# Kernel optimization log

Hardware: AMD Instinct MI355X
Metric: run time of the kernel (lower is better)

Reference implementation:

```python
import jax, jax.numpy as jnp
import numpy as np

NEG_INF = -jnp.inf


def setup_inputs() -> dict:
    key = jax.random.key(0)
    ks = jax.random.split(key, 20)
    B, N, M = 8, 1024, 128
    F_OP, F_MA, F_E, OUT, HID = 64, 64, 16, 64, 128
    inp = {
        "x": jax.random.normal(ks[0], (B, N, F_OP), dtype=jnp.float32),
        "y": jax.random.normal(ks[1], (B, M, F_MA), dtype=jnp.float32),
        "z": jax.random.normal(ks[2], (B, N, M, F_E), dtype=jnp.float32),
        "op_adj_in": jax.random.randint(ks[3], (B, N, N), 0, 2, dtype=jnp.int32),
        "ma_adj_in": jax.random.randint(ks[4], (B, N, N), 0, 2, dtype=jnp.int32),
        "op_ma_adj": jax.random.randint(ks[5], (B, N, M), 0, 2, dtype=jnp.int32),
        # learned parameters
        "weight_op": jax.random.normal(ks[6], (F_OP, OUT), dtype=jnp.float32) * 0.1,
        "weight_ma": jax.random.normal(ks[7], (F_MA, OUT), dtype=jnp.float32) * 0.1,
        "weight_edge": jax.random.normal(ks[8], (F_E, OUT), dtype=jnp.float32) * 0.1,
        "attention_op": jax.random.normal(ks[9], (1, 2 * OUT), dtype=jnp.float32) * 0.1,
        "attention_ma": jax.random.normal(ks[10], (1, 3 * OUT), dtype=jnp.float32) * 0.1,
        "w1": jax.random.normal(ks[11], (2 * OUT, HID), dtype=jnp.float32) * 0.1,
        "b1": jnp.zeros((HID,), dtype=jnp.float32),
        "w2": jax.random.normal(ks[12], (HID, HID), dtype=jnp.float32) * 0.1,
        "b2": jnp.zeros((HID,), dtype=jnp.float32),
        "wo": jax.random.normal(ks[13], (HID, OUT), dtype=jnp.float32) * 0.1,
        "bo": jnp.zeros((OUT,), dtype=jnp.float32),
    }
    return inp


def reference(x, y, z, op_adj_in, ma_adj_in, op_ma_adj,
              weight_op, weight_ma, weight_edge, attention_op, attention_ma,
              w1, b1, w2, b2, wo, bo):
    OUT = weight_op.shape[1]
    h = jnp.einsum('bni,io->bno', x, weight_op)  # [B,N,OUT]
    # all_combinations[b,i,j] = cat(h[b,j], h[b,i]); dot with attention_op splits:
    a1 = attention_op[0, :OUT]
    a2 = attention_op[0, OUT:]
    e_op = (h @ a2)[:, :, None] + (h @ a1)[:, None, :]  # [B,N,N]
    e_op = jax.nn.leaky_relu(e_op, negative_slope=0.01)

    adj = (jnp.swapaxes(op_adj_in, 1, 2) + op_adj_in
           + jnp.swapaxes(ma_adj_in, 1, 2) + ma_adj_in)  # [B,N,N]
    row_mask = jnp.all(op_ma_adj == 0, axis=-1)  # [B,N] ops with no machine link
    adj = jnp.where(row_mask[:, :, None], 1, adj)
    att = jnp.where(adj > 0, e_op, NEG_INF)
    attention_in_op = jax.nn.softmax(att, axis=2)
    h_prime_op = jnp.einsum('bij,bjo->bio', attention_in_op, h)  # [B,N,OUT]

    h_ma = jnp.einsum('bmi,io->bmo', y, weight_ma)  # [B,M,OUT]
    h_edge = jnp.einsum('bnmi,io->bnmo', z, weight_edge)  # [B,N,M,OUT]
    # cat([h_op_i, h_ma_j, h_edge_ij]) @ attention_ma split into three dots
    am1 = attention_ma[0, :OUT]
    am2 = attention_ma[0, OUT:2 * OUT]
    am3 = attention_ma[0, 2 * OUT:]
    e_ma = (h @ am1)[:, :, None] + (h_ma @ am2)[:, None, :] + h_edge @ am3  # [B,N,M]
    e_ma = jax.nn.leaky_relu(e_ma, negative_slope=0.01)

    adj2 = jnp.where(row_mask[:, :, None], 1, op_ma_adj)
    att2 = jnp.where(adj2 > 0, e_ma, NEG_INF)
    attention_in_ma = jax.nn.softmax(att2, axis=2)  # [B,N,M]
    h_ma_edge = h_ma[:, None, :, :] + h_edge  # [B,N,M,OUT]
    h_prime_ma = jnp.einsum('bnm,bnmo->bno', attention_in_ma, h_ma_edge) + h

    h_prime = jnp.concatenate([h_prime_op, h_prime_ma], axis=-1)  # [B,N,2*OUT]
    embed = jax.nn.elu(h_prime @ w1 + b1)
    embed = jax.nn.elu(embed @ w2 + b2)
    embed = embed @ wo + bo
    embed = jnp.where(row_mask[:, :, None], 0.0, embed)
    return embed
```

## Files before the change

kernel.cpp:

```cpp
#include <hip/hip_runtime.h>
#include <math.h>

#define BB 8
#define NN 1024
#define MM 128
#define FOUT 64
#define HIDN 128

#define OFF_H       0
#define OFF_HMA     524288
#define OFF_HA1     589824
#define OFF_HA2     598016
#define OFF_HAM1    606208
#define OFF_HMAAM2  614400
#define OFF_RMASK   615424
#define OFF_WAM3    623616
#define OFF_HPRIME  623632
#define OFF_UPACK   1672208
#define OFF_OPMB    1934352
#define OFF_WT1HI   1967120
#define OFF_WT1LO   1975312
#define OFF_WT2HI   1983504
#define OFF_WT2LO   1991696
#define OFF_WTOHI   1999888
#define OFF_WTOLO   2003984

typedef __attribute__((ext_vector_type(8))) short bf16x8;
typedef __attribute__((ext_vector_type(8))) unsigned short u16x8;
typedef __attribute__((ext_vector_type(4))) float f32x4;

__device__ __forceinline__ void splitbf(float v, unsigned short& h, unsigned short& l) {
    unsigned u = __float_as_uint(v);
    unsigned hb = (u + 0x7FFFu + ((u >> 16) & 1u)) >> 16;
    float hf = __uint_as_float(hb << 16);
    float lf = v - hf;
    unsigned ul = __float_as_uint(lf);
    unsigned lb = (ul + 0x7FFFu + ((ul >> 16) & 1u)) >> 16;
    h = (unsigned short)hb; l = (unsigned short)lb;
}

__global__ __launch_bounds__(256) void k1_prep(
    const float* __restrict__ x, const float* __restrict__ y,
    const int* __restrict__ op_ma_adj,
    const int* __restrict__ op_adj, const int* __restrict__ ma_adj,
    const float* __restrict__ w_op, const float* __restrict__ w_ma,
    const float* __restrict__ w_edge,
    const float* __restrict__ att_op, const float* __restrict__ att_ma,
    const float* __restrict__ w1_g, const float* __restrict__ w2_g,
    const float* __restrict__ wo_g,
    float* __restrict__ h, float* __restrict__ h_ma,
    float* __restrict__ ha1, float* __restrict__ ha2, float* __restrict__ ham1,
    float* __restrict__ hmaam2, int* __restrict__ rmask, float* __restrict__ wam3,
    unsigned* __restrict__ upack, unsigned long long* __restrict__ opmb,
    unsigned short* __restrict__ wt1hi, unsigned short* __restrict__ wt1lo,
    unsigned short* __restrict__ wt2hi, unsigned short* __restrict__ wt2lo,
    unsigned short* __restrict__ wtohi, unsigned short* __restrict__ wtolo)
{
    __shared__ float wlds[64 * 64];
    int bid = blockIdx.x;
    int t = threadIdx.x;
    int lane = t & 63;
    int wv = t >> 6;

    if (bid < 2048) {
        for (int k = t; k < 4096; k += 256) wlds[k] = w_op[k];
        __syncthreads();
        int row = bid * 4 + wv;
        float xv = x[(size_t)row * 64 + lane];
        float acc = 0.f;
        #pragma unroll
        for (int i = 0; i < 64; ++i) {
            float xi = __shfl(xv, i);
            acc += xi * wlds[i * 64 + lane];
        }
        h[(size_t)row * 64 + lane] = acc;
        float d1 = acc * att_op[lane];
        float d2 = acc * att_op[64 + lane];
        float d3 = acc * att_ma[lane];
        #pragma unroll
        for (int m = 32; m; m >>= 1) {
            d1 += __shfl_xor(d1, m);
            d2 += __shfl_xor(d2, m);
            d3 += __shfl_xor(d3, m);
        }
        int v0 = op_ma_adj[(size_t)row * 128 + lane];
        int v1 = op_ma_adj[(size_t)row * 128 + 64 + lane];
        unsigned long long w0 = __ballot(v0 != 0);
        unsigned long long w1 = __ballot(v1 != 0);
        if (lane == 0) {
            ha1[row] = d1; ha2[row] = d2; ham1[row] = d3;
            opmb[row * 2] = w0; opmb[row * 2 + 1] = w1;
            rmask[row] = ((w0 | w1) == 0ULL) ? 1 : 0;
        }
    } else if (bid < 2048 + 256) {
        for (int k = t; k < 4096; k += 256) wlds[k] = w_ma[k];
        __syncthreads();
        int row = (bid - 2048) * 4 + wv;
        float yv = y[(size_t)row * 64 + lane];
        float acc = 0.f;
        #pragma unroll
        for (int i = 0; i < 64; ++i) {
            float yi = __shfl(yv, i);
            acc += yi * wlds[i * 64 + lane];
        }
        h_ma[(size_t)row * 64 + lane] = acc;
        float d = acc * att_ma[64 + lane];
        #pragma unroll
        for (int m = 32; m; m >>= 1) d += __shfl_xor(d, m);
        if (lane == 0) hmaam2[row] = d;
    } else if (bid == 2304) {
        if (t < 16) {
            float s = 0.f;
            for (int o = 0; o < 64; ++o) s += w_edge[t * 64 + o] * att_ma[128 + o];
            wam3[t] = s;
        }
    } else if (bid < 3393) {
        unsigned* sAB = (unsigned*)wlds;
        int p = bid - 2305;
        int b = p / 136;
        int pr = p % 136;
        int I = 0;
        { int rem = pr, cnt = 16;
          while (rem >= cnt) { rem -= cnt; cnt--; I++; }
          pr = rem; }
        int J = I + pr;

        int c = t & 63, hr = (t >> 6) & 1, ts = t >> 7;
        int Ia = ts ? J : I, Ja = ts ? I : J;
        const int* opb = op_adj + (size_t)b * NN * NN + (size_t)(Ia * 64) * NN + Ja * 64;
        const int* mab = ma_adj + (size_t)b * NN * NN + (size_t)(Ia * 64) * NN + Ja * 64;
        unsigned w = 0;
        #pragma unroll 8
        for (int k = 0; k < 32; ++k) {
            int r = hr * 32 + k;
            int aval = opb[(size_t)r * NN + c] | mab[(size_t)r * NN + c];
            w |= (aval ? 1u : 0u) << k;
        }
        sAB[ts * 128 + c * 2 + hr] = w;
        __syncthreads();
        if (t < 128) {
            int r = t & 63, hh = t >> 6;
            int rw = r >> 5, rb = r & 31;
            unsigned dir1 = sAB[128 + r * 2 + hh];
            unsigned dir2 = sAB[r * 2 + hh];
            unsigned wt1 = 0, wt2 = 0;
            #pragma unroll 8
            for (int k = 0; k < 32; ++k) {
                int cc = hh * 32 + k;
                wt1 |= ((sAB[cc * 2 + rw] >> rb) & 1u) << k;
                wt2 |= ((sAB[128 + cc * 2 + rw] >> rb) & 1u) << k;
            }
            upack[((size_t)(b * NN + I * 64 + r)) * 32 + J * 2 + hh] = dir1 | wt1;
            upack[((size_t)(b * NN + J * 64 + r)) * 32 + I * 2 + hh] = dir2 | wt2;
        }
    } else {
        float (*tls)[33] = (float(*)[33])wlds;
        int p = bid - 3393;
        const float* src; unsigned short *dhi, *dlo; int KD, CD, tI, tJ;
        if (p < 16)      { src = w1_g; dhi = wt1hi; dlo = wt1lo; KD = 128; CD = 128; tI = p >> 2; tJ = p & 3; }
        else if (p < 32) { src = w2_g; dhi = wt2hi; dlo = wt2lo; KD = 128; CD = 128; tI = (p-16) >> 2; tJ = (p-16) & 3; }
        else             { src = wo_g; dhi = wtohi; dlo = wtolo; KD = 128; CD = 64;  tI = (p-32) >> 1; tJ = (p-32) & 1; }
        int k0 = tI * 32, c0 = tJ * 32;
        #pragma unroll
        for (int it = 0; it < 4; ++it) {
            int r = (t >> 5) + it * 8;
            int c = t & 31;
            tls[r][c] = src[(size_t)(k0 + r) * CD + c0 + c];
        }
        __syncthreads();
        #pragma unroll
        for (int it = 0; it < 4; ++it) {
            int c = (t >> 5) + it * 8;
            int k = t & 31;
            unsigned short hs, ls;
            splitbf(tls[k][c], hs, ls);
            dhi[(size_t)(c0 + c) * KD + k0 + k] = hs;
            dlo[(size_t)(c0 + c) * KD + k0 + k] = ls;
        }
    }
}

__global__ __launch_bounds__(256) void k2_opatt(
    const unsigned* __restrict__ upack,
    const float* __restrict__ h, const float* __restrict__ ha1,
    const float* __restrict__ ha2, const int* __restrict__ rmask,
    float* __restrict__ h_prime)
{
    __shared__ float smem[8 * 1032];
    __shared__ float ha1s[1024];
    __shared__ unsigned uw[8 * 32];
    __shared__ float denom[8];
    int bid = blockIdx.x;
    int b = bid >> 7;
    int i0 = (bid & 127) * 8;
    int t = threadIdx.x;

    uw[t & 255] = upack[((size_t)(b * NN + i0)) * 32 + t];
    for (int k = t; k < 1024; k += 256) ha1s[k] = ha1[b * NN + k];
    __syncthreads();

    int ii = t >> 5, l = t & 31;
    int i = i0 + ii;
    float ha2i = ha2[b * NN + i];
    unsigned rm = rmask[b * NN + i] ? 0xFFFFFFFFu : 0u;
    float e[32];
    #pragma unroll
    for (int it = 0; it < 32; ++it) {
        int j = l + 32 * it;
        unsigned w = uw[ii * 32 + it] | rm;
        float ev = ha2i + ha1s[j];
        ev = ev > 0.f ? ev : 0.01f * ev;
        e[it] = ((w >> l) & 1u) ? ev : -INFINITY;
    }
    float mx = -INFINITY;
    #pragma unroll
    for (int it = 0; it < 32; ++it) mx = fmaxf(mx, e[it]);
    #pragma unroll
    for (int msk = 16; msk; msk >>= 1) mx = fmaxf(mx, __shfl_xor(mx, msk));
    float s = 0.f;
    #pragma unroll
    for (int it = 0; it < 32; ++it) {
        float u = __expf(e[it] - mx);
        smem[ii * 1032 + l + 32 * it] = u;
        s += u;
    }
    #pragma unroll
    for (int msk = 16; msk; msk >>= 1) s += __shfl_xor(s, msk);
    if (l == 0) denom[ii] = s;
    __syncthreads();

    {
        int wv = t >> 6, o = t & 63;
        float acc[8];
        #pragma unroll
        for (int k = 0; k < 8; ++k) acc[k] = 0.f;
        const float* hb = h + (size_t)b * NN * 64;
        for (int jg = wv * 64; jg < wv * 64 + 64; ++jg) {
            int j = jg * 4;
            float h0 = hb[(size_t)(j + 0) * 64 + o];
            float h1 = hb[(size_t)(j + 1) * 64 + o];
            float h2 = hb[(size_t)(j + 2) * 64 + o];
            float h3 = hb[(size_t)(j + 3) * 64 + o];
            #pragma unroll
            for (int k = 0; k < 8; ++k) {
                float4 u4 = *(const float4*)&smem[k * 1032 + j];
                acc[k] += u4.x * h0 + u4.y * h1 + u4.z * h2 + u4.w * h3;
            }
        }
        __syncthreads();
        #pragma unroll
        for (int k = 0; k < 8; ++k) smem[(wv * 8 + k) * 64 + o] = acc[k];
        __syncthreads();
        int oo = t & 63;
        int k0 = t >> 6;
        for (int kk = k0; kk < 8; kk += 4) {
            float v = smem[kk * 64 + oo] + smem[(8 + kk) * 64 + oo]
                    + smem[(16 + kk) * 64 + oo] + smem[(24 + kk) * 64 + oo];
            v /= denom[kk];
            h_prime[((size_t)(b * NN + i0 + kk)) * 128 + oo] = v;
        }
    }
}

__global__ __launch_bounds__(256) void k3_maatt(
    const float* __restrict__ z, const unsigned long long* __restrict__ opmb,
    const float* __restrict__ h, const float* __restrict__ h_ma,
    const float* __restrict__ ham1, const float* __restrict__ hmaam2,
    const int* __restrict__ rmask, const float* __restrict__ wam3,
    const float* __restrict__ w_edge, float* __restrict__ h_prime)
{
    __shared__ float hma_s[128 * 64];
    __shared__ float u_s[2][128];
    __shared__ float redmx[4], redsm[4];
    __shared__ float part[2][8][16];
    __shared__ float zsum_s[2][16];
    __shared__ float hmp[2][2][64];
    __shared__ float wam3s[16];
    __shared__ float rdens[2];

    int bid = blockIdx.x;
    int b = bid >> 7;
    int n0 = (bid & 127) * 8;
    int t = threadIdx.x;
    int wvid = t >> 6;

    {
        const float4* src = (const float4*)(h_ma + (size_t)b * MM * 64);
        float4* dst = (float4*)hma_s;
        #pragma unroll
        for (int it = 0; it < 8; ++it) dst[t + 256 * it] = src[t + 256 * it];
    }
    if (t < 16) wam3s[t] = wam3[t];
    __syncthreads();

    for (int pp = 0; pp < 4; ++pp) {
        int nsel = t >> 7;
        int m = t & 127;
        int n = n0 + pp * 2 + nsel;
        int bn = b * NN + n;

        size_t zbase = ((size_t)bn * MM + m) * 16;
        float4 z0 = *(const float4*)(z + zbase);
        float4 z1 = *(const float4*)(z + zbase + 4);
        float4 z2 = *(const float4*)(z + zbase + 8);
        float4 z3 = *(const float4*)(z + zbase + 12);
        float e = ham1[bn] + hmaam2[b * MM + m];
        e += z0.x*wam3s[0] + z0.y*wam3s[1] + z0.z*wam3s[2] + z0.w*wam3s[3];
        e += z1.x*wam3s[4] + z1.y*wam3s[5] + z1.z*wam3s[6] + z1.w*wam3s[7];
        e += z2.x*wam3s[8] + z2.y*wam3s[9] + z2.z*wam3s[10] + z2.w*wam3s[11];
        e += z3.x*wam3s[12] + z3.y*wam3s[13] + z3.z*wam3s[14] + z3.w*wam3s[15];
        e = e > 0.f ? e : 0.01f * e;
        unsigned long long bits = opmb[(size_t)bn * 2 + (m >> 6)];
        int valid = rmask[bn] | (int)((bits >> (m & 63)) & 1ULL);
        e = valid ? e : -INFINITY;

        float mx = e;
        #pragma unroll
        for (int msk = 32; msk; msk >>= 1) mx = fmaxf(mx, __shfl_xor(mx, msk));
        if ((t & 63) == 0) redmx[wvid] = mx;
        __syncthreads();
        mx = fmaxf(redmx[nsel * 2], redmx[nsel * 2 + 1]);
        float uu = __expf(e - mx);
        u_s[nsel][m] = uu;
        float sv = uu;
        #pragma unroll
        for (int msk = 32; msk; msk >>= 1) sv += __shfl_xor(sv, msk);
        if ((t & 63) == 0) redsm[wvid] = sv;
        __syncthreads();
        float den = redsm[nsel * 2] + redsm[nsel * 2 + 1];
        if (m == 0) rdens[nsel] = 1.f / den;

        {
            int i = t & 15;
            int g = (t >> 4) & 7;
            int ns2 = t >> 7;
            int bn2 = b * NN + n0 + pp * 2 + ns2;
            const float* zr = z + (size_t)bn2 * MM * 16;
            float facc = 0.f;
            #pragma unroll
            for (int k = 0; k < 16; ++k) {
                int mm = g * 16 + k;
                facc += u_s[ns2][mm] * zr[(size_t)mm * 16 + i];
            }
            part[ns2][g][i] = facc;
        }
        {
            int o = t & 63;
            int q = (t >> 6) & 1;
            int ns3 = t >> 7;
            float acc = 0.f;
            #pragma unroll 8
            for (int k = 0; k < 64; ++k) {
                int mm = q * 64 + k;
                acc += u_s[ns3][mm] * hma_s[mm * 64 + o];
            }
            hmp[ns3][q][o] = acc;
        }
        __syncthreads();
        if (t < 32) {
            int ns = t >> 4, i = t & 15;
            float zs = 0.f;
            #pragma unroll
            for (int g = 0; g < 8; ++g) zs += part[ns][g][i];
            zsum_s[ns][i] = zs;
        }
        __syncthreads();
        if (t < 128) {
            int ns = t >> 6, oo = t & 63;
            int bnf = b * NN + n0 + pp * 2 + ns;
            float he = 0.f;
            #pragma unroll
            for (int i = 0; i < 16; ++i) he += zsum_s[ns][i] * w_edge[i * 64 + oo];
            float val = (hmp[ns][0][oo] + hmp[ns][1][oo] + he) * rdens[ns]
                      + h[(size_t)bnf * 64 + oo];
            h_prime[(size_t)bnf * 128 + 64 + oo] = val;
        }
        __syncthreads();
    }
}

__global__ __launch_bounds__(256) void k4_mlp(
    const float* __restrict__ hp, const int* __restrict__ rmask,
    const unsigned short* __restrict__ wt1hi, const unsigned short* __restrict__ wt1lo,
    const unsigned short* __restrict__ wt2hi, const unsigned short* __restrict__ wt2lo,
    const unsigned short* __restrict__ wtohi, const unsigned short* __restrict__ wtolo,
    const float* __restrict__ b1, const float* __restrict__ b2,
    const float* __restrict__ bo, float* __restrict__ out)
{
    __shared__ __align__(16) unsigned short Ahi0[16 * 136];
    __shared__ __align__(16) unsigned short Alo0[16 * 136];
    __shared__ __align__(16) unsigned short Ahi1[16 * 136];
    __shared__ __align__(16) unsigned short Alo1[16 * 136];
    __shared__ int rml[16];
    int t = threadIdx.x;
    int lane = t & 63;
    int wv = t >> 6;
    int row0 = blockIdx.x * 16;

    {
        int r = t >> 4;
        int cg = (t & 15) * 8;
        const float* src = hp + (size_t)(row0 + r) * 128 + cg;
        float4 v0 = *(const float4*)src;
        float4 v1 = *(const float4*)(src + 4);
        float xs[8] = {v0.x, v0.y, v0.z, v0.w, v1.x, v1.y, v1.z, v1.w};
        u16x8 hv, lv;
        #pragma unroll
        for (int j = 0; j < 8; ++j) {
            unsigned short hs, ls;
            splitbf(xs[j], hs, ls);
            hv[j] = hs; lv[j] = ls;
        }
        *(u16x8*)&Ahi0[r * 136 + cg] = hv;
        *(u16x8*)&Alo0[r * 136 + cg] = lv;
        if (t < 16) rml[t] = rmask[row0 + t];
    }
    __syncthreads();

    int arow = lane & 15;
    int kg = lane >> 4;
    int aoff = arow * 136 + kg * 8;

    {
        bf16x8 ah[4], al[4];
        #pragma unroll
        for (int ks = 0; ks < 4; ++ks) {
            ah[ks] = *(const bf16x8*)&Ahi0[aoff + ks * 32];
            al[ks] = *(const bf16x8*)&Alo0[aoff + ks * 32];
        }
        #pragma unroll
        for (int q = 0; q < 2; ++q) {
            int ct = wv + q * 4;
            int col = ct * 16 + arow;
            const unsigned short* wh = wt1hi + (size_t)col * 128 + kg * 8;
            const unsigned short* wl = wt1lo + (size_t)col * 128 + kg * 8;
            f32x4 acc = {0.f, 0.f, 0.f, 0.f};
            #pragma unroll
            for (int ks = 0; ks < 4; ++ks) {
                bf16x8 bh = *(const bf16x8*)&wh[ks * 32];
                bf16x8 bl = *(const bf16x8*)&wl[ks * 32];
                acc = __builtin_amdgcn_mfma_f32_16x16x32_bf16(ah[ks], bh, acc, 0, 0, 0);
                acc = __builtin_amdgcn_mfma_f32_16x16x32_bf16(al[ks], bh, acc, 0, 0, 0);
                acc = __builtin_amdgcn_mfma_f32_16x16x32_bf16(ah[ks], bl, acc, 0, 0, 0);
            }
            float bb = b1[col];
            #pragma unroll
            for (int r = 0; r < 4; ++r) {
                int row = kg * 4 + r;
                float v = acc[r] + bb;
                v = v > 0.f ? v : __expf(v) - 1.f;
                unsigned short hs, ls;
                splitbf(v, hs, ls);
                Ahi1[row * 136 + col] = hs;
                Alo1[row * 136 + col] = ls;
            }
        }
    }
    __syncthreads();

    {
        bf16x8 ah[4], al[4];
        #pragma unroll
        for (int ks = 0; ks < 4; ++ks) {
            ah[ks] = *(const bf16x8*)&Ahi1[aoff + ks * 32];
            al[ks] = *(const bf16x8*)&Alo1[aoff + ks * 32];
        }
        #pragma unroll
        for (int q = 0; q < 2; ++q) {
            int ct = wv + q * 4;
            int col = ct * 16 + arow;
            const unsigned short* wh = wt2hi + (size_t)col * 128 + kg * 8;
            const unsigned short* wl = wt2lo + (size_t)col * 128 + kg * 8;
            f32x4 acc = {0.f, 0.f, 0.f, 0.f};
            #pragma unroll
            for (int ks = 0; ks < 4; ++ks) {
                bf16x8 bh = *(const bf16x8*)&wh[ks * 32];
                bf16x8 bl = *(const bf16x8*)&wl[ks * 32];
                acc = __builtin_amdgcn_mfma_f32_16x16x32_bf16(ah[ks], bh, acc, 0, 0, 0);
                acc = __builtin_amdgcn_mfma_f32_16x16x32_bf16(al[ks], bh, acc, 0, 0, 0);
                acc = __builtin_amdgcn_mfma_f32_16x16x32_bf16(ah[ks], bl, acc, 0, 0, 0);
            }
            float bb = b2[col];
            #pragma unroll
            for (int r = 0; r < 4; ++r) {
                int row = kg * 4 + r;
                float v = acc[r] + bb;
                v = v > 0.f ? v : __expf(v) - 1.f;
                unsigned short hs, ls;
                splitbf(v, hs, ls);
                Ahi0[row * 136 + col] = hs;
                Alo0[row * 136 + col] = ls;
            }
        }
    }
    __syncthreads();

    {
        bf16x8 ah[4], al[4];
        #pragma unroll
        for (int ks = 0; ks < 4; ++ks) {
            ah[ks] = *(const bf16x8*)&Ahi0[aoff + ks * 32];
            al[ks] = *(const bf16x8*)&Alo0[aoff + ks * 32];
        }
        int ct = wv;
        int col = ct * 16 + arow;
        const unsigned short* wh = wtohi + (size_t)col * 128 + kg * 8;
        const unsigned short* wl = wtolo + (size_t)col * 128 + kg * 8;
        f32x4 acc = {0.f, 0.f, 0.f, 0.f};
        #pragma unroll
        for (int ks = 0; ks < 4; ++ks) {
            bf16x8 bh = *(const bf16x8*)&wh[ks * 32];
            bf16x8 bl = *(const bf16x8*)&wl[ks * 32];
            acc = __builtin_amdgcn_mfma_f32_16x16x32_bf16(ah[ks], bh, acc, 0, 0, 0);
            acc = __builtin_amdgcn_mfma_f32_16x16x32_bf16(al[ks], bh, acc, 0, 0, 0);
            acc = __builtin_amdgcn_mfma_f32_16x16x32_bf16(ah[ks], bl, acc, 0, 0, 0);
        }
        float bb = bo[col];
        #pragma unroll
        for (int r = 0; r < 4; ++r) {
            int row = kg * 4 + r;
            float v = acc[r] + bb;
            out[(size_t)(row0 + row) * 64 + col] = rml[row] ? 0.f : v;
        }
    }
}

extern "C" void kernel_launch(void* const* d_in, const int* in_sizes, int n_in,
                              void* d_out, int out_size, void* d_ws, size_t ws_size,
                              hipStream_t stream) {
    const float* x      = (const float*)d_in[0];
    const float* y      = (const float*)d_in[1];
    const float* z      = (const float*)d_in[2];
    const int*   op_adj = (const int*)d_in[3];
    const int*   ma_adj = (const int*)d_in[4];
    const int*   opma   = (const int*)d_in[5];
    const float* w_op   = (const float*)d_in[6];
    const float* w_ma   = (const float*)d_in[7];
    const float* w_edge = (const float*)d_in[8];
    const float* att_op = (const float*)d_in[9];
    const float* att_ma = (const float*)d_in[10];
    const float* w1     = (const float*)d_in[11];
    const float* b1     = (const float*)d_in[12];
    const float* w2     = (const float*)d_in[13];
    const float* b2     = (const float*)d_in[14];
    const float* wo     = (const float*)d_in[15];
    const float* bo     = (const float*)d_in[16];
    float* out = (float*)d_out;

    float* ws = (float*)d_ws;
    float* h       = ws + OFF_H;
    float* h_ma    = ws + OFF_HMA;
    float* ha1     = ws + OFF_HA1;
    float* ha2     = ws + OFF_HA2;
    float* ham1    = ws + OFF_HAM1;
    float* hmaam2  = ws + OFF_HMAAM2;
    int*   rmask   = (int*)(ws + OFF_RMASK);
    float* wam3    = ws + OFF_WAM3;
    float* h_prime = ws + OFF_HPRIME;
    unsigned* upack = (unsigned*)(ws + OFF_UPACK);
    unsigned long long* opmb = (unsigned long long*)(ws + OFF_OPMB);
    unsigned short* wt1hi = (unsigned short*)(ws + OFF_WT1HI);
    unsigned short* wt1lo = (unsigned short*)(ws + OFF_WT1LO);
    unsigned short* wt2hi = (unsigned short*)(ws + OFF_WT2HI);
    unsigned short* wt2lo = (unsigned short*)(ws + OFF_WT2LO);
    unsigned short* wtohi = (unsigned short*)(ws + OFF_WTOHI);
    unsigned short* wtolo = (unsigned short*)(ws + OFF_WTOLO);

    k1_prep<<<2048 + 256 + 1 + 1088 + 40, 256, 0, stream>>>(
        x, y, opma, op_adj, ma_adj, w_op, w_ma, w_edge, att_op, att_ma,
        w1, w2, wo,
        h, h_ma, ha1, ha2, ham1, hmaam2, rmask, wam3, upack, opmb,
        wt1hi, wt1lo, wt2hi, wt2lo, wtohi, wtolo);

    k2_opatt<<<1024, 256, 0, stream>>>(
        upack, h, ha1, ha2, rmask, h_prime);

    k3_maatt<<<1024, 256, 0, stream>>>(
        z, opmb, h, h_ma, ham1, hmaam2, rmask, wam3, w_edge, h_prime);

    k4_mlp<<<512, 256, 0, stream>>>(
        h_prime, rmask, wt1hi, wt1lo, wt2hi, wt2lo, wtohi, wtolo,
        b1, b2, bo, out);
}
```

Measured before the change: 91.55 us.

## Use bf16 MFMA with hi/lo split for op-attention aggregation

k1_prep now also writes a transposed, bf16 hi/lo-split copy of h. k2_opatt handles 16 rows per block instead of 8, rounds the unnormalised softmax weights to bf16 into a swizzled LDS tile, and computes P·h with 16x16x32 bf16 MFMA (hi and lo passes). This replaces the scalar FP32 FMA loop and halves the grid. In exchange, the attention weights are rounded to bf16, which reduces accuracy, and k1 does extra scattered 2-byte stores.

```diff
diff --git a/kernel.cpp b/kernel.cpp
--- a/kernel.cpp
+++ b/kernel.cpp
@@ -24,6 +24,8 @@
 #define OFF_WT2LO   1991696
 #define OFF_WTOHI   1999888
 #define OFF_WTOLO   2003984
+#define OFF_HTHI    2008080
+#define OFF_HTLO    2270224
 
 typedef __attribute__((ext_vector_type(8))) short bf16x8;
 typedef __attribute__((ext_vector_type(8))) unsigned short u16x8;
@@ -54,7 +56,8 @@
     unsigned* __restrict__ upack, unsigned long long* __restrict__ opmb,
     unsigned short* __restrict__ wt1hi, unsigned short* __restrict__ wt1lo,
     unsigned short* __restrict__ wt2hi, unsigned short* __restrict__ wt2lo,
-    unsigned short* __restrict__ wtohi, unsigned short* __restrict__ wtolo)
+    unsigned short* __restrict__ wtohi, unsigned short* __restrict__ wtolo,
+    unsigned short* __restrict__ hthi, unsigned short* __restrict__ htlo)
 {
     __shared__ float wlds[64 * 64];
     int bid = blockIdx.x;
@@ -74,6 +77,12 @@
             acc += xi * wlds[i * 64 + lane];
         }
         h[(size_t)row * 64 + lane] = acc;
+        {
+            unsigned short hs, ls;
+            splitbf(acc, hs, ls);
+            size_t tb = ((size_t)((row >> 10) * 64 + lane)) * 1024 + (row & 1023);
+            hthi[tb] = hs; htlo[tb] = ls;
+        }
         float d1 = acc * att_op[lane];
         float d2 = acc * att_op[64 + lane];
         float d3 = acc * att_ma[lane];
@@ -182,82 +191,91 @@
 
 __global__ __launch_bounds__(256) void k2_opatt(
     const unsigned* __restrict__ upack,
-    const float* __restrict__ h, const float* __restrict__ ha1,
-    const float* __restrict__ ha2, const int* __restrict__ rmask,
-    float* __restrict__ h_prime)
+    const unsigned short* __restrict__ hthi,
+    const unsigned short* __restrict__ htlo,
+    const float* __restrict__ ha1, const float* __restrict__ ha2,
+    const int* __restrict__ rmask, float* __restrict__ h_prime)
 {
-    __shared__ float smem[8 * 1032];
+    __shared__ __align__(16) unsigned short Pl[16 * 1024];
     __shared__ float ha1s[1024];
-    __shared__ unsigned uw[8 * 32];
-    __shared__ float denom[8];
+    __shared__ unsigned uws[512];
+    __shared__ float rdeninv[16];
     int bid = blockIdx.x;
-    int b = bid >> 7;
-    int i0 = (bid & 127) * 8;
+    int b = bid >> 6;
+    int i0 = (bid & 63) << 4;
     int t = threadIdx.x;
 
-    uw[t & 255] = upack[((size_t)(b * NN + i0)) * 32 + t];
-    for (int k = t; k < 1024; k += 256) ha1s[k] = ha1[b * NN + k];
+    {
+        size_t ub = (size_t)(b * NN + i0) * 32;
+        uws[t] = upack[ub + t];
+        uws[t + 256] = upack[ub + t + 256];
+    }
+    ha1s[t] = ha1[b * NN + t];
+    ha1s[t + 256] = ha1[b * NN + t + 256];
+    ha1s[t + 512] = ha1[b * NN + t + 512];
+    ha1s[t + 768] = ha1[b * NN + t + 768];
     __syncthreads();
 
-    int ii = t >> 5, l = t & 31;
-    int i = i0 + ii;
-    float ha2i = ha2[b * NN + i];
-    unsigned rm = rmask[b * NN + i] ? 0xFFFFFFFFu : 0u;
-    float e[32];
-    #pragma unroll
-    for (int it = 0; it < 32; ++it) {
-        int j = l + 32 * it;
-        unsigned w = uw[ii * 32 + it] | rm;
-        float ev = ha2i + ha1s[j];
-        ev = ev > 0.f ? ev : 0.01f * ev;
-        e[it] = ((w >> l) & 1u) ? ev : -INFINITY;
-    }
-    float mx = -INFINITY;
-    #pragma unroll
-    for (int it = 0; it < 32; ++it) mx = fmaxf(mx, e[it]);
-    #pragma unroll
-    for (int msk = 16; msk; msk >>= 1) mx = fmaxf(mx, __shfl_xor(mx, msk));
-    float s = 0.f;
-    #pragma unroll
-    for (int it = 0; it < 32; ++it) {
-        float u = __expf(e[it] - mx);
-        smem[ii * 1032 + l + 32 * it] = u;
-        s += u;
-    }
-    #pragma unroll
-    for (int msk = 16; msk; msk >>= 1) s += __shfl_xor(s, msk);
-    if (l == 0) denom[ii] = s;
+    {
+        int row = t >> 4, q = t & 15;
+        int bn = b * NN + i0 + row;
+        float ha2i = ha2[bn];
+        unsigned rm = rmask[bn] ? 0xFFFFFFFFu : 0u;
+
+        float mx = -INFINITY;
+        #pragma unroll 8
+        for (int jj = 0; jj < 64; ++jj) {
+            int j = q + (jj << 4);
+            float ev = ha2i + ha1s[j];
+            ev = ev > 0.f ? ev : 0.01f * ev;
+            unsigned w = uws[row * 32 + (j >> 5)] | rm;
+            if ((w >> (j & 31)) & 1u) mx = fmaxf(mx, ev);
+        }
+        #pragma unroll
+        for (int m = 1; m < 16; m <<= 1) mx = fmaxf(mx, __shfl_xor(mx, m));
+
+        float s = 0.f;
+        #pragma unroll 4
+        for (int jj = 0; jj < 64; ++jj) {
+            int j = q + (jj << 4);
+            float ev = ha2i + ha1s[j];
+            ev = ev > 0.f ? ev : 0.01f * ev;
+            unsigned w = uws[row * 32 + (j >> 5)] | rm;
+            float u = ((w >> (j & 31)) & 1u) ? __expf(ev - mx) : 0.f;
+            s += u;
+            unsigned ub = __float_as_uint(u);
+            unsigned short pb = (unsigned short)((ub + 0x7FFFu + ((ub >> 16) & 1u)) >> 16);
+            unsigned byteoff = ((unsigned)(row * 2048 + j * 2)) ^ ((unsigned)((row & 7) << 4));
+            *(unsigned short*)((char*)Pl + byteoff) = pb;
+        }
+        #pragma unroll
+        for (int m = 1; m < 16; m <<= 1) s += __shfl_xor(s, m);
+        if (q == 0) rdeninv[row] = 1.f / s;
+    }
     __syncthreads();
 
     {
-        int wv = t >> 6, o = t & 63;
-        float acc[8];
-        #pragma unroll
-        for (int k = 0; k < 8; ++k) acc[k] = 0.f;
-        const float* hb = h + (size_t)b * NN * 64;
-        for (int jg = wv * 64; jg < wv * 64 + 64; ++jg) {
-            int j = jg * 4;
-            float h0 = hb[(size_t)(j + 0) * 64 + o];
-            float h1 = hb[(size_t)(j + 1) * 64 + o];
-            float h2 = hb[(size_t)(j + 2) * 64 + o];
-            float h3 = hb[(size_t)(j + 3) * 64 + o];
-            #pragma unroll
-            for (int k = 0; k < 8; ++k) {
-                float4 u4 = *(const float4*)&smem[k * 1032 + j];
-                acc[k] += u4.x * h0 + u4.y * h1 + u4.z * h2 + u4.w * h3;
-            }
-        }
-        __syncthreads();
-        #pragma unroll
-        for (int k = 0; k < 8; ++k) smem[(wv * 8 + k) * 64 + o] = acc[k];
-        __syncthreads();
-        int oo = t & 63;
-        int k0 = t >> 6;
-        for (int kk = k0; kk < 8; kk += 4) {
-            float v = smem[kk * 64 + oo] + smem[(8 + kk) * 64 + oo]
-                    + smem[(16 + kk) * 64 + oo] + smem[(24 + kk) * 64 + oo];
-            v /= denom[kk];
-            h_prime[((size_t)(b * NN + i0 + kk)) * 128 + oo] = v;
+        int lane = t & 63, wvv = t >> 6;
+        int arow = lane & 15, kg = lane >> 4;
+        int col = wvv * 16 + arow;
+        const unsigned short* bhp = hthi + ((size_t)(b * 64 + col)) * 1024;
+        const unsigned short* blp = htlo + ((size_t)(b * 64 + col)) * 1024;
+        f32x4 acc = {0.f, 0.f, 0.f, 0.f};
+        #pragma unroll 8
+        for (int kst = 0; kst < 32; ++kst) {
+            unsigned cc = ((unsigned)(kst * 4 + kg)) ^ ((unsigned)(arow & 7));
+            bf16x8 pa = *(const bf16x8*)((char*)Pl + arow * 2048 + cc * 16);
+            bf16x8 vh = *(const bf16x8*)&bhp[kst * 32 + kg * 8];
+            bf16x8 vl = *(const bf16x8*)&blp[kst * 32 + kg * 8];
+            acc = __builtin_amdgcn_mfma_f32_16x16x32_bf16(pa, vh, acc, 0, 0, 0);
+            acc = __builtin_amdgcn_mfma_f32_16x16x32_bf16(pa, vl, acc, 0, 0, 0);
+        }
+        size_t base = (size_t)(b * NN + i0);
+        #pragma unroll
+        for (int r = 0; r < 4; ++r) {
+            int orow = kg * 4 + r;
+            float v = acc[r] * rdeninv[orow];
+            h_prime[(base + orow) * 128 + col] = v;
         }
     }
 }
@@ -565,15 +583,17 @@
     unsigned short* wt2lo = (unsigned short*)(ws + OFF_WT2LO);
     unsigned short* wtohi = (unsigned short*)(ws + OFF_WTOHI);
     unsigned short* wtolo = (unsigned short*)(ws + OFF_WTOLO);
+    unsigned short* hthi  = (unsigned short*)(ws + OFF_HTHI);
+    unsigned short* htlo  = (unsigned short*)(ws + OFF_HTLO);
 
     k1_prep<<<2048 + 256 + 1 + 1088 + 40, 256, 0, stream>>>(
         x, y, opma, op_adj, ma_adj, w_op, w_ma, w_edge, att_op, att_ma,
         w1, w2, wo,
         h, h_ma, ha1, ha2, ham1, hmaam2, rmask, wam3, upack, opmb,
-        wt1hi, wt1lo, wt2hi, wt2lo, wtohi, wtolo);
-
-    k2_opatt<<<1024, 256, 0, stream>>>(
-        upack, h, ha1, ha2, rmask, h_prime);
+        wt1hi, wt1lo, wt2hi, wt2lo, wtohi, wtolo, hthi, htlo);
+
+    k2_opatt<<<512, 256, 0, stream>>>(
+        upack, hthi, htlo, ha1, ha2, rmask, h_prime);
 
     k3_maatt<<<1024, 256, 0, stream>>>(
         z, opmb, h, h_ma, ham1, hmaam2, rmask, wam3, w_edge, h_prime);
```

Measured after the change: 87.44 us. 1.05x faster.
